# Kernel optimization log

Hardware: AMD Instinct MI355X
Metric: run time of the kernel (lower is better)

The kernel has to match this reference:

```python
import jax, jax.numpy as jnp
import numpy as np

B, T, F, D, H, DFF, L = 8, 1024, 64, 512, 8, 2048, 3
DH = D // H
PERIODS = np.array([16, 256, 4096], np.int32)
CMS_LRS = np.array([0.01, 0.001, 0.0001], np.float32)
TITANS_LR = 0.01
TITANS_CLIP = 0.1


def layernorm(x, w, b):
    m = x.mean(-1, keepdims=True)
    v = x.var(-1, keepdims=True)
    return (x - m) * jax.lax.rsqrt(v + 1e-5) * w + b


def setup_inputs() -> dict:
    key = jax.random.key(0)
    ks = jax.random.split(key, 40)
    f32 = jnp.float32
    def rn(i, shape, s=0.02):
        return jax.random.normal(ks[i], shape, f32) * s
    inp = {
        'x': jax.random.normal(ks[0], (B, T, F), f32),
        'titans_W': jnp.zeros((D, D), f32),
        'cms_summary': jnp.zeros((L, D), f32),
        'cms_buf_sum': jnp.zeros((L, D), f32),
        'cms_count': jnp.zeros((L,), jnp.int32),
        'cms_step': jnp.zeros((L,), jnp.int32),
        'in_norm_w': jnp.ones((F,), f32), 'in_norm_b': jnp.zeros((F,), f32),
        'in_proj_W': rn(1, (D, F)), 'in_proj_b': jnp.zeros((D,), f32),
        'W_base': rn(2, (D, D), 0.01),
        'tit_out_W': rn(3, (D, D)), 'tit_out_b': jnp.zeros((D,), f32),
        'gate_W': rn(4, (L, D, D)), 'gate_b': jnp.zeros((L, D), f32),
        'comb_W': rn(5, (D, L * D)), 'comb_b': jnp.zeros((D,), f32),
        'n1_w': jnp.ones((D,), f32), 'n1_b': jnp.zeros((D,), f32),
        'qkv_W': rn(6, (3 * D, D)), 'qkv_b': jnp.zeros((3 * D,), f32),
        'ao_W': rn(7, (D, D)), 'ao_b': jnp.zeros((D,), f32),
        'n2_w': jnp.ones((D,), f32), 'n2_b': jnp.zeros((D,), f32),
        'f1_W': rn(8, (DFF, D)), 'f1_b': jnp.zeros((DFF,), f32),
        'f2_W': rn(9, (D, DFF)), 'f2_b': jnp.zeros((D,), f32),
        'fn_w': jnp.ones((D,), f32), 'fn_b': jnp.zeros((D,), f32),
        'head_W': rn(10, (1, D)), 'head_b': jnp.zeros((1,), f32),
    }
    return inp


def cms_tick_all(means, summary, buf_sum, count, step, gate_W, gate_b):
    """Sequential tick over T timesteps, vectorized over the L levels.
    means: [T, D] batch-mean of final hidden at each timestep."""
    periods = jnp.asarray(PERIODS)
    lrs = jnp.asarray(CMS_LRS)
    def step_fn(carry, m):
        summ, bs, cnt, stp = carry
        bs = bs + m[None, :]              # [L, D]
        cnt = cnt + 1
        stp = stp + 1
        fire = cnt >= periods              # [L]
        acc = bs / cnt.astype(bs.dtype)[:, None]
        g = jax.nn.sigmoid(jnp.einsum('lij,lj->li', gate_W, acc) + gate_b)
        new_summ = jnp.where(fire[:, None], (1.0 - lrs)[:, None] * summ + lrs[:, None] * g * acc, summ)
        bs = jnp.where(fire[:, None], jnp.zeros_like(bs), bs)
        cnt = jnp.where(fire, jnp.zeros_like(cnt), cnt)
        return (new_summ, bs, cnt, stp), None
    (summary, buf_sum, count, step), _ = jax.lax.scan(step_fn, (summary, buf_sum, count, step), means)
    return summary, buf_sum, count, step


def reference(x, titans_W, cms_summary, cms_buf_sum, cms_count, cms_step,
              in_norm_w, in_norm_b, in_proj_W, in_proj_b,
              W_base, tit_out_W, tit_out_b,
              gate_W, gate_b, comb_W, comb_b,
              n1_w, n1_b, qkv_W, qkv_b, ao_W, ao_b,
              n2_w, n2_b, f1_W, f1_b, f2_W, f2_b,
              fn_w, fn_b, head_W, head_b):
    # input norm + projection: [B,T,F] -> [B,T,D]
    h = layernorm(x, in_norm_w, in_norm_b) @ in_proj_W.T + in_proj_b
    # Titans fast-weight read
    W = W_base + titans_W
    tit = (h @ W.T) @ tit_out_W.T + tit_out_b
    # Titans fast-weight update (detached in the original)
    hs = jax.lax.stop_gradient(h)
    target = hs.mean(axis=1)               # [B, D]
    query = hs[:, -1, :]                   # [B, D]
    pred_m = query @ titans_W.T
    err = (target - pred_m).mean(axis=0)   # [D]
    grad = jnp.outer(err, query.mean(axis=0))
    gn = jnp.linalg.norm(grad)
    grad = jnp.where(gn > TITANS_CLIP, grad * (TITANS_CLIP / gn), grad)
    new_W = titans_W + TITANS_LR * grad
    h = h + tit
    # CMS residual from current summaries: concat [L*D] -> combine -> [D]
    cms_out = cms_summary.reshape(L * D) @ comb_W.T + comb_b
    h = h + cms_out                        # broadcast over [B,T,D]
    # transformer block (pre-norm, causal MHA)
    hn = layernorm(h, n1_w, n1_b)
    qkv = hn @ qkv_W.T + qkv_b
    q, k, v = jnp.split(qkv, 3, axis=-1)
    def to_heads(t):
        return t.reshape(B, T, H, DH).transpose(0, 2, 1, 3)
    q, k, v = to_heads(q), to_heads(k), to_heads(v)
    scores = jnp.einsum('bhqd,bhkd->bhqk', q, k) / np.sqrt(DH).astype(np.float32)
    causal = jnp.triu(jnp.ones((T, T), bool), 1)
    scores = jnp.where(causal, -jnp.inf, scores)
    attn = jax.nn.softmax(scores, axis=-1)
    ao = jnp.einsum('bhqk,bhkd->bhqd', attn, v).transpose(0, 2, 1, 3).reshape(B, T, D)
    h = h + ao @ ao_W.T + ao_b
    hn2 = layernorm(h, n2_w, n2_b)
    h = h + jax.nn.gelu(hn2 @ f1_W.T + f1_b, approximate=False) @ f2_W.T + f2_b
    h = layernorm(h, fn_w, fn_b)
    pred = (h @ head_W.T + head_b).squeeze(-1)   # [B, T]
    # CMS tick over all T steps (detached in the original)
    means = jax.lax.stop_gradient(h).mean(axis=0)  # [T, D]
    ns, nb, nc, nt = cms_tick_all(means, cms_summary, cms_buf_sum, cms_count, cms_step, gate_W, gate_b)
    return pred, new_W, ns, nb, nc, nt
```

## Files before the change

### kernel.cpp

```cpp
#include <hip/hip_runtime.h>
#include <hip/hip_bf16.h>
#include <math.h>

#define Bdim 8
#define Tdim 1024
#define Fdim 64
#define Ddim 512
#define Lcms 3

#define OFF_PRED 0
#define OFF_W    8192
#define OFF_NS   270336
#define OFF_NB   271872
#define OFF_NC   273408
#define OFF_NT   273411

typedef __hip_bfloat16 bf16;
typedef __attribute__((ext_vector_type(8))) short s8;
typedef __attribute__((ext_vector_type(4))) float f4;

__device__ __forceinline__ float b2f(bf16 v){ return __bfloat162float(v); }
__device__ __forceinline__ bf16  f2b(float v){ return __float2bfloat16(v); }
__device__ __forceinline__ short fb16(float v){ bf16 t = __float2bfloat16(v); return *reinterpret_cast<short*>(&t); }
__device__ __forceinline__ float sh2f(short s){ bf16 t = *reinterpret_cast<bf16*>(&s); return __bfloat162float(t); }
__device__ __forceinline__ float toF(float v){ return v; }
__device__ __forceinline__ float toF(bf16 v){ return __bfloat162float(v); }
template<typename T> __device__ __forceinline__ T fromF(float v);
template<> __device__ __forceinline__ float fromF<float>(float v){ return v; }
template<> __device__ __forceinline__ bf16  fromF<bf16 >(float v){ return f2b(v); }

__device__ __forceinline__ f4 mfma16(s8 a, s8 b, f4 c){
  return __builtin_amdgcn_mfma_f32_16x16x32_bf16(a, b, c, 0, 0, 0);
}

__device__ __forceinline__ void gload16(const bf16* g, bf16* l){
  __builtin_amdgcn_global_load_lds(
      (const __attribute__((address_space(1))) unsigned*)g,
      (__attribute__((address_space(3))) unsigned*)l, 16, 0, 0);
}

__device__ __forceinline__ float gelu_fast(float x){
  float z2 = 1.5957691216f*(x + 0.044715f*x*x*x);
  z2 = fminf(fmaxf(z2, -18.f), 18.f);
  return x / (1.f + __expf(-z2));
}

template<typename TW>
__device__ __forceinline__ void front_misc(int blk, int tid,
    const TW* x, const TW* nw, const TW* nb_, bf16* xn,
    const TW* Wbse, const TW* tW, bf16* Wout,
    const TW* summ, const TW* combW, const TW* combb, float* outv){
  if (blk < 2048){
    int row = blk*4 + (tid>>6);
    int lane = tid & 63;
    float v = toF(x[(size_t)row*Fdim + lane]);
    float s = v, s2 = v*v;
    #pragma unroll
    for (int off=32; off; off>>=1){ s += __shfl_down(s,off); s2 += __shfl_down(s2,off); }
    s = __shfl(s, 0); s2 = __shfl(s2, 0);
    float mu = s*(1.f/64.f);
    float var = s2*(1.f/64.f) - mu*mu;
    float rstd = rsqrtf(var + 1e-5f);
    xn[(size_t)row*Fdim + lane] = f2b((v-mu)*rstd*toF(nw[lane]) + toF(nb_[lane]));
  } else if (blk < 3072){
    int i = (blk-2048)*256 + tid;
    Wout[i] = f2b(toF(Wbse[i]) + toF(tW[i]));
  } else {
    __shared__ float s_s[Lcms*Ddim];
    for (int i=tid;i<Lcms*Ddim;i+=256) s_s[i] = toF(summ[i]);
    __syncthreads();
    int wave = tid>>6, lane = tid&63;
    int d = (blk-3072)*4 + wave;
    const TW* wr = combW + (size_t)d*(Lcms*Ddim);
    float a = 0.f;
    for (int j=lane;j<Lcms*Ddim;j+=64) a += s_s[j]*toF(wr[j]);
    #pragma unroll
    for (int off=32; off; off>>=1) a += __shfl_down(a,off);
    if (lane==0) outv[d] = a + toF(combb[d]);
  }
}
__global__ __launch_bounds__(256) void k_front(
    const void* s0, const void* s1, const void* s2, const void* s3,
    const void* s4, const void* s5, const void* s6, const void* s7,
    const void* s8v, const void* s9, const void* s10, const void* s11,
    const void* s12, const void* s13,
    bf16* __restrict__ dst, const unsigned* __restrict__ w1, int* __restrict__ flag,
    const int* __restrict__ cnt, int* __restrict__ params,
    const void* x, const void* nw, const void* nb_, bf16* xn,
    const void* Wbse, const void* tW, bf16* Wout,
    const void* summ, const void* combW, const void* combb, float* outv,
    float* __restrict__ colsum){
  bool isbf = (w1[0] == 0x3F803F80u);
  int blk = blockIdx.x, tid = threadIdx.x;
  if (blk==0 && tid==0){
    flag[0] = isbf ? 1 : 0;
    const int P[3] = {16,256,4096};
    for (int l=0;l<3;l++){
      int c0 = cnt[l];
      int t1 = P[l] - c0 - 1; if (t1 < 0) t1 = 0;
      int K = (t1 >= Tdim) ? 0 : 1 + (Tdim-1-t1)/P[l];
      params[l*4+0]=t1; params[l*4+1]=K; params[l*4+2]=c0+t1+1; params[l*4+3]=c0;
    }
  }
  if (blk == 1){
    for (int i=tid; i<Bdim*Ddim; i+=256) colsum[i] = 0.f;
  }
  if (blk < 1024){
    const void* srcs[14] = {s0,s1,s2,s3,s4,s5,s6,s7,s8v,s9,s10,s11,s12,s13};
    const int   ns[14]   = {262144,512,786432,1536,262144,512,1048576,2048,1048576,512,
                            32768,512,786432,1536};
    const int gstride = 1024*256;
    int gid = blk*256 + tid;
    int base = 0;
    #pragma unroll
    for (int s=0;s<14;s++){
      int n = ns[s];
      if (isbf){
        const short* sp = (const short*)srcs[s]; short* dp = (short*)(dst+base);
        for (int i=gid;i<n;i+=gstride) dp[i] = sp[i];
      } else {
        const float* sp = (const float*)srcs[s];
        for (int i=gid;i<n;i+=gstride) dst[base+i] = f2b(sp[i]);
      }
      base += n;
    }
  } else {
    int b2 = blk - 1024;
    if (isbf) front_misc<bf16>(b2, tid, (const bf16*)x,(const bf16*)nw,(const bf16*)nb_,xn,
                               (const bf16*)Wbse,(const bf16*)tW,Wout,
                               (const bf16*)summ,(const bf16*)combW,(const bf16*)combb,outv);
    else      front_misc<float>(b2, tid, (const float*)x,(const float*)nw,(const float*)nb_,xn,
                               (const float*)Wbse,(const float*)tW,Wout,
                               (const float*)summ,(const float*)combW,(const float*)combb,outv);
  }
}

__global__ void k_tq2(const bf16* __restrict__ h, const float* __restrict__ colsum,
    float* __restrict__ target, float* __restrict__ query){
  int i = blockIdx.x*256 + threadIdx.x;
  int b = i>>9, d = i&511;
  target[i] = colsum[i]*(1.f/(float)Tdim);
  query[i]  = b2f(h[((size_t)b*Tdim + (Tdim-1))*Ddim + d]);
}

template<typename TW>
__device__ __forceinline__ void titans_err_impl(const float* target, const float* query,
    const TW* tW, float* err, float* qmean){
  int wave = threadIdx.x>>6, lane = threadIdx.x&63;
  int d = blockIdx.x*4 + wave;
  const TW* wr = tW + (size_t)d*Ddim;
  float s = 0.f;
  #pragma unroll
  for (int b=0;b<Bdim;b++){
    const float* q = query + b*Ddim;
    float p = 0.f;
    for (int j=lane;j<Ddim;j+=64) p += q[j]*toF(wr[j]);
    s += p;
  }
  #pragma unroll
  for (int off=32; off; off>>=1) s += __shfl_down(s,off);
  if (lane==0){
    float e=0.f, qm=0.f;
    #pragma unroll
    for (int b=0;b<Bdim;b++){ e += target[b*Ddim+d]; qm += query[b*Ddim+d]; }
    err[d]   = (e - s)*(1.f/(float)Bdim);
    qmean[d] = qm*(1.f/(float)Bdim);
  }
}
__global__ __launch_bounds__(256) void k_titans_err(const float* target, const float* query,
    const void* tW, float* err, float* qmean, const int* flg){
  if (*flg) titans_err_impl<bf16>(target,query,(const bf16*)tW,err,qmean);
  else      titans_err_impl<float>(target,query,(const float*)tW,err,qmean);
}

template<typename TW>
__device__ __forceinline__ void new_W_impl(const TW* tW, const float* err, const float* qmean,
    TW* outW){
  int tid = threadIdx.x;
  float a = err[tid]*err[tid] + err[tid+256]*err[tid+256];
  float b = qmean[tid]*qmean[tid] + qmean[tid+256]*qmean[tid+256];
  #pragma unroll
  for (int off=32; off; off>>=1){ a += __shfl_down(a,off); b += __shfl_down(b,off); }
  __shared__ float sa[4], sb[4];
  int lane = tid & 63, wid = tid >> 6;
  if (lane==0){ sa[wid]=a; sb[wid]=b; }
  __syncthreads();
  float A = sa[0]+sa[1]+sa[2]+sa[3];
  float Bq= sb[0]+sb[1]+sb[2]+sb[3];
  float gn = sqrtf(A*Bq);
  float sf = 0.01f * (gn > 0.1f ? 0.1f/gn : 1.0f);
  int i = blockIdx.x*256 + tid;
  int r = i >> 9, c = i & 511;
  outW[i] = fromF<TW>(toF(tW[i]) + sf*err[r]*qmean[c]);
}
__global__ __launch_bounds__(256) void k_new_W(const void* tW, const float* err,
    const float* qmean, void* out, const int* flg){
  if (*flg) new_W_impl<bf16>((const bf16*)tW, err, qmean, ((bf16*)out)+OFF_W);
  else      new_W_impl<float>((const float*)tW, err, qmean, ((float*)out)+OFF_W);
}

template<int MODE, int DEPTH>
__global__ __launch_bounds__(512) void gemm_mfma(const bf16* __restrict__ A,
    const bf16* __restrict__ Bw, const bf16* __restrict__ bias,
    const float* __restrict__ colvec, bf16* __restrict__ Cout,
    const bf16* __restrict__ resid, int M, int N, int K, float* __restrict__ colsum){
  __shared__ __align__(16) bf16 As[DEPTH][128*32];
  __shared__ __align__(16) bf16 Bs[DEPTH][128*32];
  int tid = threadIdx.x, wave = tid>>6, lane = tid&63, quad = lane>>4, l16 = lane&15;
  int row0 = blockIdx.x*128, col0 = blockIdx.y*128;
  int wr = (wave>>2)*64, wc = (wave&3)*32;
  int srow = wave*16 + (lane>>2);
  int scol = (((lane&3) ^ ((lane>>3)&3)))*8;
  int rswz = (quad ^ ((l16>>1)&3))*8;
  f4 acc[8] = {};
  int niter = K >> 5;
  #define STAGE(bu, k0) { \
    gload16(A  + (size_t)(row0 + srow)*K + (k0) + scol, &As[bu][wave*512 + lane*8]); \
    gload16(Bw + (size_t)(col0 + srow)*K + (k0) + scol, &Bs[bu][wave*512 + lane*8]); \
  }
  STAGE(0, 0)
  if (DEPTH >= 3 && niter > 1) STAGE(1, 32)
  if (DEPTH >= 4 && niter > 2) STAGE(2, 64)
  for (int k=0; k<niter; k++){
    int bu = k & (DEPTH-1);
    if (DEPTH == 2){
      if (k+1 < niter){
        STAGE((k+1)&1, (k+1)<<5)
        asm volatile("s_waitcnt vmcnt(2)" ::: "memory");
      } else {
        asm volatile("s_waitcnt vmcnt(0)" ::: "memory");
      }
    } else {
      if (k+3 < niter){
        STAGE((k+3)&3, (k+3)<<5)
        asm volatile("s_waitcnt vmcnt(6)" ::: "memory");
      } else if (k+2 < niter){
        asm volatile("s_waitcnt vmcnt(4)" ::: "memory");
      } else if (k+1 < niter){
        asm volatile("s_waitcnt vmcnt(2)" ::: "memory");
      } else {
        asm volatile("s_waitcnt vmcnt(0)" ::: "memory");
      }
    }
    __builtin_amdgcn_s_barrier();
    s8 af[4], bfv[2];
    #pragma unroll
    for (int i=0;i<4;i++) af[i]  = *reinterpret_cast<const s8*>(&As[bu][(wr + i*16 + l16)*32 + rswz]);
    #pragma unroll
    for (int j=0;j<2;j++) bfv[j] = *reinterpret_cast<const s8*>(&Bs[bu][(wc + j*16 + l16)*32 + rswz]);
    #pragma unroll
    for (int i=0;i<4;i++)
      #pragma unroll
      for (int j=0;j<2;j++)
        acc[i*2+j] = mfma16(af[i], bfv[j], acc[i*2+j]);
    asm volatile("s_waitcnt lgkmcnt(0)" ::: "memory");
    __builtin_amdgcn_s_barrier();
  }
  #undef STAGE
  float cs[2] = {0.f, 0.f};
  #pragma unroll
  for (int i=0;i<4;i++){
    #pragma unroll
    for (int j=0;j<2;j++){
      int n = col0 + wc + j*16 + l16;
      f4 a = acc[i*2+j];
      #pragma unroll
      for (int r=0;r<4;r++){
        int m = row0 + wr + i*16 + quad*4 + r;
        float v = a[r];
        if (MODE & 1) v += b2f(bias[n]);
        if (MODE & 8) v += colvec[n];
        if (MODE & 4) v = gelu_fast(v);
        if (MODE & 2) v += b2f(resid[(size_t)m*Ddim + n]);
        Cout[(size_t)m*N + n] = f2b(v);
        if (MODE & 16) cs[j] += v;
      }
    }
  }
  if (MODE & 16){
    int bIdx = blockIdx.x >> 3;
    #pragma unroll
    for (int j=0;j<2;j++){
      float c = cs[j];
      c += __shfl_xor(c, 16);
      c += __shfl_xor(c, 32);
      if (quad == 0)
        atomicAdd(&colsum[bIdx*Ddim + col0 + wc + j*16 + l16], c);
    }
  }
}

template<typename TW>
__device__ __forceinline__ void ln_impl(const bf16* in, const TW* w, const TW* b, bf16* outp){
  int row = blockIdx.x;
  const bf16* r = in + (size_t)row*Ddim;
  int tid = threadIdx.x;
  float v0 = b2f(r[tid]), v1 = b2f(r[tid + 256]);
  float s = v0+v1, s2 = v0*v0 + v1*v1;
  #pragma unroll
  for (int off=32; off; off>>=1){ s += __shfl_down(s,off); s2 += __shfl_down(s2,off); }
  __shared__ float sa[4], sb[4];
  int lane = tid & 63, wid = tid >> 6;
  if (lane==0){ sa[wid]=s; sb[wid]=s2; }
  __syncthreads();
  float ts  = sa[0]+sa[1]+sa[2]+sa[3];
  float ts2 = sb[0]+sb[1]+sb[2]+sb[3];
  float mu = ts*(1.f/(float)Ddim);
  float var = ts2*(1.f/(float)Ddim) - mu*mu;
  float rstd = rsqrtf(var + 1e-5f);
  outp[(size_t)row*Ddim + tid]       = f2b((v0-mu)*rstd*toF(w[tid])     + toF(b[tid]));
  outp[(size_t)row*Ddim + tid + 256] = f2b((v1-mu)*rstd*toF(w[tid+256]) + toF(b[tid+256]));
}
__global__ __launch_bounds__(256) void k_ln(const bf16* in, const void* w, const void* b,
    bf16* outp, const int* flg){
  if (*flg) ln_impl<bf16>(in,(const bf16*)w,(const bf16*)b,outp);
  else      ln_impl<float>(in,(const float*)w,(const float*)b,outp);
}

template<typename TW>
__device__ __forceinline__ void ln_hm_impl(const bf16* in, const TW* w, const TW* b,
    bf16* outp, const TW* hw, const TW* hb, TW* pred, float* means){
  int t = blockIdx.x;
  int tid = threadIdx.x, wave = tid>>6, lane = tid&63;
  int d0 = lane*8;
  __shared__ float msum[4][Ddim];
  float wv[8], bv[8], hwv[8];
  #pragma unroll
  for (int j=0;j<8;j++){ wv[j]=toF(w[d0+j]); bv[j]=toF(b[d0+j]); hwv[j]=toF(hw[d0+j]); }
  float hb0 = toF(hb[0]);
  float osum[8] = {0,0,0,0,0,0,0,0};
  #pragma unroll
  for (int rr=0; rr<2; rr++){
    int bb = wave*2 + rr;
    size_t row = (size_t)bb*Tdim + t;
    s8 raw = *reinterpret_cast<const s8*>(in + row*Ddim + d0);
    float v[8];
    float s=0.f, s2=0.f;
    #pragma unroll
    for (int j=0;j<8;j++){ v[j]=sh2f(raw[j]); s+=v[j]; s2+=v[j]*v[j]; }
    #pragma unroll
    for (int off=32; off; off>>=1){ s += __shfl_down(s,off); s2 += __shfl_down(s2,off); }
    s = __shfl(s,0); s2 = __shfl(s2,0);
    float mu = s*(1.f/(float)Ddim);
    float var = s2*(1.f/(float)Ddim) - mu*mu;
    float rstd = rsqrtf(var + 1e-5f);
    float sp = 0.f;
    s8 ob;
    #pragma unroll
    for (int j=0;j<8;j++){
      float o = (v[j]-mu)*rstd*wv[j] + bv[j];
      ob[j] = fb16(o);
      sp += o*hwv[j];
      osum[j] += o;
    }
    *reinterpret_cast<s8*>(outp + row*Ddim + d0) = ob;
    #pragma unroll
    for (int off=32; off; off>>=1) sp += __shfl_down(sp,off);
    if (lane==0) pred[row] = fromF<TW>(sp + hb0);
  }
  #pragma unroll
  for (int j=0;j<8;j++) msum[wave][d0+j] = osum[j];
  __syncthreads();
  for (int d=tid; d<Ddim; d+=256)
    means[(size_t)t*Ddim + d] = (msum[0][d]+msum[1][d]+msum[2][d]+msum[3][d])*(1.f/8.f);
}
__global__ __launch_bounds__(256) void k_ln_hm(const bf16* in, const void* w, const void* b,
    bf16* outp, const void* hw, const void* hb, void* out, float* means, const int* flg){
  if (*flg) ln_hm_impl<bf16>(in,(const bf16*)w,(const bf16*)b,outp,
                             (const bf16*)hw,(const bf16*)hb,((bf16*)out)+OFF_PRED,means);
  else      ln_hm_impl<float>(in,(const float*)w,(const float*)b,outp,
                             (const float*)hw,(const float*)hb,((float*)out)+OFF_PRED,means);
}

__global__ __launch_bounds__(256) void k_attn_mfma(const bf16* __restrict__ qkv,
                                                   bf16* __restrict__ ao){
  int blk = blockIdx.x;
  int bh = blk & 63;
  int qt = 15 - (blk >> 6);
  int head = bh & 7, b = bh >> 3;
  __shared__ __align__(16) bf16 Ks[2][64][72];
  __shared__ __align__(16) unsigned Vt4[2][64*36];
  __shared__ __align__(16) bf16 Ps[4][16][72];
  int tid = threadIdx.x, wave = tid>>6, lane = tid&63, quad = lane>>4, l16 = lane&15;
  int q0w = qt*64 + wave*16;
  const bf16* basep = qkv + (size_t)b*Tdim*1536 + head*64;
  s8 qf0 = *reinterpret_cast<const s8*>(basep + (size_t)(q0w+l16)*1536 + quad*8);
  s8 qf1 = *reinterpret_cast<const s8*>(basep + (size_t)(q0w+l16)*1536 + 32 + quad*8);
  f4 o[4] = {{0,0,0,0},{0,0,0,0},{0,0,0,0},{0,0,0,0}};
  float m_r[4] = {-3.0e38f,-3.0e38f,-3.0e38f,-3.0e38f};
  float l_r[4] = {0.f,0.f,0.f,0.f};
  int key_s = tid>>3, dgk = (tid&7)*8;
  int vp = tid>>3, dgv = (tid&7)*8;
  int vu4 = (((vp>>2) ^ (tid&7)) & 7)*4 + (vp&3);
  int nch = qt + 1;
  s8 kr0[2], kr1[2], vra[2], vrb[2];
  {
    const bf16* kp = basep + (size_t)key_s*1536 + 512 + dgk;
    kr0[0] = *reinterpret_cast<const s8*>(kp);
    kr1[0] = *reinterpret_cast<const s8*>(kp + (size_t)32*1536);
    const bf16* vpa = basep + (size_t)(2*vp)*1536 + 1024 + dgv;
    vra[0] = *reinterpret_cast<const s8*>(vpa);
    vrb[0] = *reinterpret_cast<const s8*>(vpa + 1536);
    if (1 < nch){
      const bf16* kp1 = basep + (size_t)(64+key_s)*1536 + 512 + dgk;
      kr0[1] = *reinterpret_cast<const s8*>(kp1);
      kr1[1] = *reinterpret_cast<const s8*>(kp1 + (size_t)32*1536);
      const bf16* vpa1 = basep + (size_t)(64 + 2*vp)*1536 + 1024 + dgv;
      vra[1] = *reinterpret_cast<const s8*>(vpa1);
      vrb[1] = *reinterpret_cast<const s8*>(vpa1 + 1536);
    }
  }
  auto do_chunk = [&](int ch, int bu){
    f4 sc4[4] = {{0,0,0,0},{0,0,0,0},{0,0,0,0},{0,0,0,0}};
    #pragma unroll
    for (int t=0;t<4;t++){
      sc4[t] = mfma16(qf0, *reinterpret_cast<const s8*>(&Ks[bu][t*16+l16][quad*8]),    sc4[t]);
      sc4[t] = mfma16(qf1, *reinterpret_cast<const s8*>(&Ks[bu][t*16+l16][32+quad*8]), sc4[t]);
    }
    int key0 = ch*64 + l16;
    #pragma unroll
    for (int r=0;r<4;r++){
      int qrow = q0w + quad*4 + r;
      float a0 = (key0      <= qrow) ? sc4[0][r]*0.125f : -3.0e38f;
      float a1 = (key0 + 16 <= qrow) ? sc4[1][r]*0.125f : -3.0e38f;
      float a2 = (key0 + 32 <= qrow) ? sc4[2][r]*0.125f : -3.0e38f;
      float a3 = (key0 + 48 <= qrow) ? sc4[3][r]*0.125f : -3.0e38f;
      float mx = fmaxf(fmaxf(a0,a1), fmaxf(a2,a3));
      mx = fmaxf(mx, __shfl_xor(mx,1)); mx = fmaxf(mx, __shfl_xor(mx,2));
      mx = fmaxf(mx, __shfl_xor(mx,4)); mx = fmaxf(mx, __shfl_xor(mx,8));
      float mnew = fmaxf(m_r[r], mx);
      float al = __expf(m_r[r]-mnew); m_r[r] = mnew;
      float p0 = __expf(a0-mnew), p1 = __expf(a1-mnew);
      float p2 = __expf(a2-mnew), p3 = __expf(a3-mnew);
      float rs = (p0+p1)+(p2+p3);
      rs += __shfl_xor(rs,1); rs += __shfl_xor(rs,2);
      rs += __shfl_xor(rs,4); rs += __shfl_xor(rs,8);
      l_r[r] = l_r[r]*al + rs;
      o[0][r]*=al; o[1][r]*=al; o[2][r]*=al; o[3][r]*=al;
      int prow = quad*4+r;
      *reinterpret_cast<short*>(&Ps[wave][prow][l16])    = fb16(p0);
      *reinterpret_cast<short*>(&Ps[wave][prow][16+l16]) = fb16(p1);
      *reinterpret_cast<short*>(&Ps[wave][prow][32+l16]) = fb16(p2);
      *reinterpret_cast<short*>(&Ps[wave][prow][48+l16]) = fb16(p3);
    }
    asm volatile("s_waitcnt lgkmcnt(0)" ::: "memory");
    s8 pf0 = *reinterpret_cast<const s8*>(&Ps[wave][l16][quad*8]);
    s8 pf1 = *reinterpret_cast<const s8*>(&Ps[wave][l16][32+quad*8]);
    #pragma unroll
    for (int j=0;j<4;j++){
      int d = j*16 + l16;
      int swz = (d>>3) & 7;
      s8 b0 = *reinterpret_cast<const s8*>(&Vt4[bu][d*36 + ((quad   ^ swz))*4]);
      s8 b1 = *reinterpret_cast<const s8*>(&Vt4[bu][d*36 + (((4+quad)^ swz))*4]);
      o[j] = mfma16(pf0, b0, o[j]);
      o[j] = mfma16(pf1, b1, o[j]);
    }
  };
  for (int ch0=0; ch0<nch; ch0+=2){
    #pragma unroll
    for (int s=0;s<2;s++){
      if (ch0+s < nch){
        *reinterpret_cast<s8*>(&Ks[s][key_s][dgk])    = kr0[s];
        *reinterpret_cast<s8*>(&Ks[s][32+key_s][dgk]) = kr1[s];
        #pragma unroll
        for (int j=0;j<8;j++){
          unsigned w = (unsigned)(unsigned short)vra[s][j] | ((unsigned)(unsigned short)vrb[s][j] << 16);
          Vt4[s][(dgv+j)*36 + vu4] = w;
        }
      }
    }
    __syncthreads();
    #pragma unroll
    for (int s=0;s<2;s++){
      int chn = ch0 + 2 + s;
      if (chn < nch){
        const bf16* kp = basep + (size_t)(chn*64+key_s)*1536 + 512 + dgk;
        kr0[s] = *reinterpret_cast<const s8*>(kp);
        kr1[s] = *reinterpret_cast<const s8*>(kp + (size_t)32*1536);
        const bf16* vpa = basep + (size_t)(chn*64 + 2*vp)*1536 + 1024 + dgv;
        vra[s] = *reinterpret_cast<const s8*>(vpa);
        vrb[s] = *reinterpret_cast<const s8*>(vpa + 1536);
      }
    }
    do_chunk(ch0, 0);
    if (ch0+1 < nch) do_chunk(ch0+1, 1);
    if (ch0+2 < nch) __syncthreads();
  }
  #pragma unroll
  for (int r=0;r<4;r++){
    float inv = 1.f/l_r[r];
    size_t rowb = (size_t)(b*Tdim + q0w + quad*4 + r)*Ddim + head*64;
    ao[rowb + l16]      = f2b(o[0][r]*inv);
    ao[rowb + 16 + l16] = f2b(o[1][r]*inv);
    ao[rowb + 32 + l16] = f2b(o[2][r]*inv);
    ao[rowb + 48 + l16] = f2b(o[3][r]*inv);
  }
}

template<typename TW>
__device__ __forceinline__ void cms_acc_impl(const float* means, const TW* bs0,
    const int* params, float* acc, bf16* acch, float* tailtmp){
  int tid = threadIdx.x;
  if (blockIdx.x < 384){
    int l = blockIdx.x>>7, k = blockIdx.x&127;
    int K = params[l*4+1];
    if (k >= K){
      for (int d=tid; d<Ddim; d+=256) acch[((size_t)l*128+k)*Ddim + d] = f2b(0.f);
      return;
    }
    int t1 = params[l*4], cnt0 = params[l*4+2];
    const int P[3] = {16,256,4096};
    int lo = (k==0) ? 0 : t1 + (k-1)*P[l] + 1;
    int hi = t1 + k*P[l];
    float inv = 1.f/((k==0) ? (float)cnt0 : (float)P[l]);
    int lane = tid&63, strip = tid>>6;
    __shared__ float red[4][Ddim];
    float4 a0 = {0,0,0,0}, a1 = {0,0,0,0};
    for (int t=lo+strip; t<=hi; t+=4){
      const float4* row = (const float4*)(means + (size_t)t*Ddim);
      float4 v0 = row[lane], v1 = row[lane+64];
      a0.x+=v0.x; a0.y+=v0.y; a0.z+=v0.z; a0.w+=v0.w;
      a1.x+=v1.x; a1.y+=v1.y; a1.z+=v1.z; a1.w+=v1.w;
    }
    ((float4*)red[strip])[lane]    = a0;
    ((float4*)red[strip])[lane+64] = a1;
    __syncthreads();
    for (int d=tid; d<Ddim; d+=256){
      float s = red[0][d]+red[1][d]+red[2][d]+red[3][d];
      if (k==0) s += toF(bs0[l*Ddim+d]);
      float v = s*inv;
      acc[((size_t)l*65+k)*Ddim + d] = v;
      acch[((size_t)l*128+k)*Ddim + d] = f2b(v);
    }
  } else {
    int bb = blockIdx.x - 384;
    int l = bb>>5, chunk = bb&31;
    int t1 = params[l*4], K = params[l*4+1];
    const int P[3] = {16,256,4096};
    int lo = (K==0) ? 0 : t1 + (K-1)*P[l] + 1;
    int f = tid & 127, strip = tid >> 7;
    int tbeg = chunk*32, tend = tbeg + 32;
    if (tbeg < lo) tbeg = lo;
    float4 a = {0,0,0,0};
    for (int t=tbeg+strip; t<tend; t+=2){
      float4 v = ((const float4*)(means + (size_t)t*Ddim))[f];
      a.x+=v.x; a.y+=v.y; a.z+=v.z; a.w+=v.w;
    }
    __shared__ float4 redt[2][128];
    redt[strip][f] = a;
    __syncthreads();
    if (strip==0){
      float4 b = redt[1][f];
      a.x+=b.x; a.y+=b.y; a.z+=b.z; a.w+=b.w;
      ((float4*)(tailtmp + ((size_t)l*32 + chunk)*Ddim))[f] = a;
    }
  }
}
__global__ __launch_bounds__(256) void k_cms_acc(const float* means, const void* bs0,
    const int* params, float* acc, bf16* acch, float* tailtmp, const int* flg){
  if (*flg) cms_acc_impl<bf16>(means,(const bf16*)bs0,params,acc,acch,tailtmp);
  else      cms_acc_impl<float>(means,(const float*)bs0,params,acc,acch,tailtmp);
}

__global__ __launch_bounds__(256) void k_cms_gate_mfma(const bf16* __restrict__ accbh,
    const bf16* __restrict__ wg, const bf16* __restrict__ wgb, float* __restrict__ g){
  int l = blockIdx.y;
  const bf16* A  = accbh + (size_t)l*128*Ddim;
  const bf16* Bw = wg    + (size_t)l*Ddim*Ddim;
  __shared__ __align__(16) bf16 As[128*32];
  __shared__ __align__(16) bf16 Bs[128*32];
  int tid = threadIdx.x, wave = tid>>6, lane = tid&63, quad = lane>>4, l16 = lane&15;
  int col0 = blockIdx.x*128;
  int wr = (wave>>1)*64, wc = (wave&1)*64;
  int srow = lane>>2, scol = (lane&3)*8;
  f4 acc[16] = {};
  for (int k0=0; k0<Ddim; k0+=32){
    __syncthreads();
    #pragma unroll
    for (int it=0; it<2; it++){
      int c = wave*2 + it;
      gload16(A  + (size_t)(c*16 + srow)*Ddim + k0 + scol, &As[c*512 + lane*8]);
      gload16(Bw + (size_t)(col0 + c*16 + srow)*Ddim + k0 + scol, &Bs[c*512 + lane*8]);
    }
    __syncthreads();
    s8 af[4], bfv[4];
    #pragma unroll
    for (int i=0;i<4;i++) af[i]  = *reinterpret_cast<const s8*>(&As[(wr + i*16 + l16)*32 + quad*8]);
    #pragma unroll
    for (int j=0;j<4;j++) bfv[j] = *reinterpret_cast<const s8*>(&Bs[(wc + j*16 + l16)*32 + quad*8]);
    #pragma unroll
    for (int i=0;i<4;i++)
      #pragma unroll
      for (int j=0;j<4;j++)
        acc[i*4+j] = mfma16(af[i], bfv[j], acc[i*4+j]);
  }
  #pragma unroll
  for (int i=0;i<4;i++){
    #pragma unroll
    for (int j=0;j<4;j++){
      int n = col0 + wc + j*16 + l16;
      f4 a = acc[i*4+j];
      #pragma unroll
      for (int r=0;r<4;r++){
        int m = wr + i*16 + quad*4 + r;
        if (m < 65){
          float v = a[r] + b2f(wgb[l*Ddim + n]);
          g[((size_t)l*65 + m)*Ddim + n] = 1.f/(1.f + __expf(-v));
        }
      }
    }
  }
}

template<typename TW>
__device__ __forceinline__ void cms_final_impl(const float* acc, const float* g,
    const float* tailtmp, const TW* summ0, const TW* bs0, const int* params,
    const int* step0, TW* out){
  int l = blockIdx.x;
  int t1 = params[l*4], K = params[l*4+1], c0 = params[l*4+3];
  const int P[3] = {16,256,4096};
  const float LR[3] = {0.01f,0.001f,0.0001f};
  float lr = LR[l];
  for (int d=threadIdx.x; d<Ddim; d+=256){
    float s = toF(summ0[l*Ddim + d]);
    for (int k=0;k<K;k++)
      s = (1.f-lr)*s + lr*g[((size_t)l*65+k)*Ddim+d]*acc[((size_t)l*65+k)*Ddim+d];
    out[OFF_NS + l*Ddim + d] = fromF<TW>(s);
    float nbv = (K==0) ? toF(bs0[l*Ddim+d]) : 0.f;
    #pragma unroll
    for (int c=0;c<32;c++) nbv += tailtmp[((size_t)l*32+c)*Ddim + d];
    out[OFF_NB + l*Ddim + d] = fromF<TW>(nbv);
  }
  if (threadIdx.x==0){
    int nc = (K==0) ? c0 + Tdim : (Tdim-1 - (t1 + (K-1)*P[l]));
    out[OFF_NC + l] = fromF<TW>((float)nc);
    out[OFF_NT + l] = fromF<TW>((float)(step0[l] + Tdim));
  }
}
__global__ __launch_bounds__(256) void k_cms_final(const float* acc, const float* g,
    const float* tailtmp, const void* summ0, const void* bs0, const int* params,
    const int* step0, void* out, const int* flg){
  if (*flg) cms_final_impl<bf16>(acc,g,tailtmp,(const bf16*)summ0,(const bf16*)bs0,params,step0,(bf16*)out);
  else      cms_final_impl<float>(acc,g,tailtmp,(const float*)summ0,(const float*)bs0,params,step0,(float*)out);
}

extern "C" void kernel_launch(void* const* d_in, const int* in_sizes, int n_in,
                              void* d_out, int out_size, void* d_ws, size_t ws_size,
                              hipStream_t stream) {
  (void)in_sizes; (void)n_in; (void)out_size; (void)ws_size;
  const void* x           = d_in[0];
  const void* titansW     = d_in[1];
  const void* cms_summary = d_in[2];
  const void* cms_bufsum  = d_in[3];
  const int*  cms_count   = (const int*)d_in[4];
  const int*  cms_step    = (const int*)d_in[5];
  const void* in_norm_w   = d_in[6];
  const void* in_norm_b   = d_in[7];
  const void* in_proj_W   = d_in[8];
  const void* in_proj_b   = d_in[9];
  const void* W_base      = d_in[10];
  const void* tit_out_W   = d_in[11];
  const void* tit_out_b   = d_in[12];
  const void* gate_W      = d_in[13];
  const void* gate_b      = d_in[14];
  const void* comb_W      = d_in[15];
  const void* comb_b      = d_in[16];
  const void* n1_w        = d_in[17];
  const void* n1_b        = d_in[18];
  const void* qkv_W       = d_in[19];
  const void* qkv_b       = d_in[20];
  const void* ao_W        = d_in[21];
  const void* ao_b        = d_in[22];
  const void* n2_w        = d_in[23];
  const void* n2_b        = d_in[24];
  const void* f1_W        = d_in[25];
  const void* f1_b        = d_in[26];
  const void* f2_W        = d_in[27];
  const void* f2_b        = d_in[28];
  const void* fn_w        = d_in[29];
  const void* fn_b        = d_in[30];
  const void* head_W      = d_in[31];
  const void* head_b      = d_in[32];

  char* u8 = (char*)d_ws;
  bf16*  h     = (bf16*)(u8 + 0);
  bf16*  hnA   = (bf16*)(u8 + 8388608);
  bf16*  big   = (bf16*)(u8 + 16777216);
  bf16*  xn    = big;
  bf16*  tmid  = big + (size_t)8192*1536;
  float* means = (float*)(u8 + 50331648);
  bf16*  Wb    = (bf16*)(u8 + 52428800);
  bf16*  wall  = (bf16*)(u8 + 52953088);
  bf16*  wtit  = wall;
  bf16*  wtitb = wall + 262144;
  bf16*  wqkv  = wall + 262656;
  bf16*  wqkvb = wall + 1049088;
  bf16*  wao   = wall + 1050624;
  bf16*  waob  = wall + 1312768;
  bf16*  wf1   = wall + 1313280;
  bf16*  wf1b  = wall + 2361856;
  bf16*  wf2   = wall + 2363904;
  bf16*  wf2b  = wall + 3412480;
  bf16*  wproj = wall + 3412992;
  bf16*  wprojb= wall + 3445760;
  bf16*  wgate = wall + 3446272;
  bf16*  wgateb= wall + 4232704;
  float* target= (float*)(u8 + 61421568);
  float* query = (float*)(u8 + 61437952);
  float* errv  = (float*)(u8 + 61454336);
  float* qmean = (float*)(u8 + 61456384);
  float* cmsout= (float*)(u8 + 61458944);
  float* accb  = (float*)(u8 + 61460992);
  float* gbuf  = (float*)(u8 + 61860352);
  bf16*  accbh = (bf16*) (u8 + 62259712);
  int*   params= (int*)  (u8 + 62652928);
  int*   dflag = (int*)  (u8 + 62652992);
  float* colsum= (float*)(u8 + 62659584);
  float* tailtmp=(float*)(u8 + 63183872);

  k_front<<<4224, 256, 0, stream>>>(tit_out_W, tit_out_b, qkv_W, qkv_b, ao_W, ao_b,
                                    f1_W, f1_b, f2_W, f2_b, in_proj_W, in_proj_b,
                                    gate_W, gate_b, wall, (const unsigned*)in_norm_w,
                                    dflag, cms_count, params,
                                    x, in_norm_w, in_norm_b, xn,
                                    W_base, titansW, Wb,
                                    cms_summary, comb_W, comb_b, cmsout, colsum);
  gemm_mfma<17,2><<<dim3(64,4), 512, 0, stream>>>(xn, wproj, wprojb, nullptr, h, nullptr, 8192, 512, 64, colsum);
  k_tq2<<<16, 256, 0, stream>>>(h, colsum, target, query);
  k_titans_err<<<128, 256, 0, stream>>>(target, query, titansW, errv, qmean, dflag);
  k_new_W<<<1024, 256, 0, stream>>>(titansW, errv, qmean, d_out, dflag);
  gemm_mfma<0,4><<<dim3(64,4), 512, 0, stream>>>(h, Wb, nullptr, nullptr, tmid, nullptr, 8192, 512, 512, nullptr);
  gemm_mfma<11,4><<<dim3(64,4), 512, 0, stream>>>(tmid, wtit, wtitb, cmsout, h, h, 8192, 512, 512, nullptr);
  k_ln<<<8192, 256, 0, stream>>>(h, n1_w, n1_b, hnA, dflag);
  gemm_mfma<1,2><<<dim3(64,12), 512, 0, stream>>>(hnA, wqkv, wqkvb, nullptr, big, nullptr, 8192, 1536, 512, nullptr);
  k_attn_mfma<<<1024, 256, 0, stream>>>(big, tmid);
  gemm_mfma<3,4><<<dim3(64,4), 512, 0, stream>>>(tmid, wao, waob, nullptr, h, h, 8192, 512, 512, nullptr);
  k_ln<<<8192, 256, 0, stream>>>(h, n2_w, n2_b, hnA, dflag);
  gemm_mfma<5,2><<<dim3(64,16), 512, 0, stream>>>(hnA, wf1, wf1b, nullptr, big, nullptr, 8192, 2048, 512, nullptr);
  gemm_mfma<3,4><<<dim3(64,4), 512, 0, stream>>>(big, wf2, wf2b, nullptr, h, h, 8192, 512, 2048, nullptr);
  k_ln_hm<<<1024, 256, 0, stream>>>(h, fn_w, fn_b, hnA, head_W, head_b, d_out, means, dflag);
  k_cms_acc<<<480, 256, 0, stream>>>(means, cms_bufsum, params, accb, accbh, tailtmp, dflag);
  k_cms_gate_mfma<<<dim3(4,3), 256, 0, stream>>>(accbh, wgate, wgateb, gbuf);
  k_cms_final<<<Lcms, 256, 0, stream>>>(accb, gbuf, tailtmp, cms_summary, cms_bufsum, params, cms_step, d_out, dflag);
}
```

Measured before the change: 432.0 us.

## Add 64-row-tile GEMM for N=512 layers and fold tq2 into titans_err

Adds a new MFMA GEMM kernel with 64x128 block tiles and double-buffered LDS staging. It is used for the four N=512 GEMMs, launching 512 blocks instead of 256 so more of the GPU's compute units are busy. It also removes the small k_tq2 kernel and lets titans_err read the last-timestep rows of h and colsum directly, saving one launch and a round trip through memory. The smaller tiles mean less operand reuse per block and more total global loads.

```diff
diff --git a/kernel.cpp b/kernel.cpp
--- a/kernel.cpp
+++ b/kernel.cpp
@@ -135,16 +135,8 @@
   }
 }
 
-__global__ void k_tq2(const bf16* __restrict__ h, const float* __restrict__ colsum,
-    float* __restrict__ target, float* __restrict__ query){
-  int i = blockIdx.x*256 + threadIdx.x;
-  int b = i>>9, d = i&511;
-  target[i] = colsum[i]*(1.f/(float)Tdim);
-  query[i]  = b2f(h[((size_t)b*Tdim + (Tdim-1))*Ddim + d]);
-}
-
 template<typename TW>
-__device__ __forceinline__ void titans_err_impl(const float* target, const float* query,
+__device__ __forceinline__ void titans_err_impl(const bf16* h, const float* colsum,
     const TW* tW, float* err, float* qmean){
   int wave = threadIdx.x>>6, lane = threadIdx.x&63;
   int d = blockIdx.x*4 + wave;
@@ -152,9 +144,9 @@
   float s = 0.f;
   #pragma unroll
   for (int b=0;b<Bdim;b++){
-    const float* q = query + b*Ddim;
+    const bf16* q = h + ((size_t)b*Tdim + (Tdim-1))*Ddim;
     float p = 0.f;
-    for (int j=lane;j<Ddim;j+=64) p += q[j]*toF(wr[j]);
+    for (int j=lane;j<Ddim;j+=64) p += b2f(q[j])*toF(wr[j]);
     s += p;
   }
   #pragma unroll
@@ -162,15 +154,18 @@
   if (lane==0){
     float e=0.f, qm=0.f;
     #pragma unroll
-    for (int b=0;b<Bdim;b++){ e += target[b*Ddim+d]; qm += query[b*Ddim+d]; }
+    for (int b=0;b<Bdim;b++){
+      e  += colsum[b*Ddim+d]*(1.f/(float)Tdim);
+      qm += b2f(h[((size_t)b*Tdim + (Tdim-1))*Ddim + d]);
+    }
     err[d]   = (e - s)*(1.f/(float)Bdim);
     qmean[d] = qm*(1.f/(float)Bdim);
   }
 }
-__global__ __launch_bounds__(256) void k_titans_err(const float* target, const float* query,
+__global__ __launch_bounds__(256) void k_titans_err(const bf16* h, const float* colsum,
     const void* tW, float* err, float* qmean, const int* flg){
-  if (*flg) titans_err_impl<bf16>(target,query,(const bf16*)tW,err,qmean);
-  else      titans_err_impl<float>(target,query,(const float*)tW,err,qmean);
+  if (*flg) titans_err_impl<bf16>(h,colsum,(const bf16*)tW,err,qmean);
+  else      titans_err_impl<float>(h,colsum,(const float*)tW,err,qmean);
 }
 
 template<typename TW>
@@ -286,6 +281,71 @@
       c += __shfl_xor(c, 32);
       if (quad == 0)
         atomicAdd(&colsum[bIdx*Ddim + col0 + wc + j*16 + l16], c);
+    }
+  }
+}
+
+template<int MODE>
+__global__ __launch_bounds__(512) void gemm_mfma64(const bf16* __restrict__ A,
+    const bf16* __restrict__ Bw, const bf16* __restrict__ bias,
+    const float* __restrict__ colvec, bf16* __restrict__ Cout,
+    const bf16* __restrict__ resid, int M, int N, int K){
+  __shared__ __align__(16) bf16 As[2][64*32];
+  __shared__ __align__(16) bf16 Bs[2][128*32];
+  int tid = threadIdx.x, wave = tid>>6, lane = tid&63, quad = lane>>4, l16 = lane&15;
+  int row0 = blockIdx.x*64, col0 = blockIdx.y*128;
+  int wr = (wave>>2)*32, wc = (wave&3)*32;
+  int srow = lane>>2;
+  int scol = (((lane&3) ^ ((lane>>3)&3)))*8;
+  int rswz = (quad ^ ((l16>>1)&3))*8;
+  f4 acc[4] = {};
+  int niter = K >> 5;
+  #define STAGE64(bu, k0) { \
+    if (wave < 4) \
+      gload16(A + (size_t)(row0 + wave*16 + srow)*K + (k0) + scol, &As[bu][wave*512 + lane*8]); \
+    gload16(Bw + (size_t)(col0 + wave*16 + srow)*K + (k0) + scol, &Bs[bu][wave*512 + lane*8]); \
+  }
+  STAGE64(0, 0)
+  for (int k=0; k<niter; k++){
+    int bu = k & 1;
+    if (k+1 < niter){
+      STAGE64((k+1)&1, (k+1)<<5)
+      if (wave < 4) asm volatile("s_waitcnt vmcnt(2)" ::: "memory");
+      else          asm volatile("s_waitcnt vmcnt(1)" ::: "memory");
+    } else {
+      asm volatile("s_waitcnt vmcnt(0)" ::: "memory");
+    }
+    __builtin_amdgcn_s_barrier();
+    s8 af[2], bfv[2];
+    #pragma unroll
+    for (int i=0;i<2;i++) af[i]  = *reinterpret_cast<const s8*>(&As[bu][(wr + i*16 + l16)*32 + rswz]);
+    #pragma unroll
+    for (int j=0;j<2;j++) bfv[j] = *reinterpret_cast<const s8*>(&Bs[bu][(wc + j*16 + l16)*32 + rswz]);
+    #pragma unroll
+    for (int i=0;i<2;i++)
+      #pragma unroll
+      for (int j=0;j<2;j++)
+        acc[i*2+j] = mfma16(af[i], bfv[j], acc[i*2+j]);
+    asm volatile("s_waitcnt lgkmcnt(0)" ::: "memory");
+    __builtin_amdgcn_s_barrier();
+  }
+  #undef STAGE64
+  #pragma unroll
+  for (int i=0;i<2;i++){
+    #pragma unroll
+    for (int j=0;j<2;j++){
+      int n = col0 + wc + j*16 + l16;
+      f4 a = acc[i*2+j];
+      #pragma unroll
+      for (int r=0;r<4;r++){
+        int m = row0 + wr + i*16 + quad*4 + r;
+        float v = a[r];
+        if (MODE & 1) v += b2f(bias[n]);
+        if (MODE & 8) v += colvec[n];
+        if (MODE & 4) v = gelu_fast(v);
+        if (MODE & 2) v += b2f(resid[(size_t)m*Ddim + n]);
+        Cout[(size_t)m*N + n] = f2b(v);
+      }
     }
   }
 }
@@ -705,8 +765,6 @@
   bf16*  wprojb= wall + 3445760;
   bf16*  wgate = wall + 3446272;
   bf16*  wgateb= wall + 4232704;
-  float* target= (float*)(u8 + 61421568);
-  float* query = (float*)(u8 + 61437952);
   float* errv  = (float*)(u8 + 61454336);
   float* qmean = (float*)(u8 + 61456384);
   float* cmsout= (float*)(u8 + 61458944);
@@ -726,18 +784,17 @@
                                     W_base, titansW, Wb,
                                     cms_summary, comb_W, comb_b, cmsout, colsum);
   gemm_mfma<17,2><<<dim3(64,4), 512, 0, stream>>>(xn, wproj, wprojb, nullptr, h, nullptr, 8192, 512, 64, colsum);
-  k_tq2<<<16, 256, 0, stream>>>(h, colsum, target, query);
-  k_titans_err<<<128, 256, 0, stream>>>(target, query, titansW, errv, qmean, dflag);
+  k_titans_err<<<128, 256, 0, stream>>>(h, colsum, titansW, errv, qmean, dflag);
   k_new_W<<<1024, 256, 0, stream>>>(titansW, errv, qmean, d_out, dflag);
-  gemm_mfma<0,4><<<dim3(64,4), 512, 0, stream>>>(h, Wb, nullptr, nullptr, tmid, nullptr, 8192, 512, 512, nullptr);
-  gemm_mfma<11,4><<<dim3(64,4), 512, 0, stream>>>(tmid, wtit, wtitb, cmsout, h, h, 8192, 512, 512, nullptr);
+  gemm_mfma64<0><<<dim3(128,4), 512, 0, stream>>>(h, Wb, nullptr, nullptr, tmid, nullptr, 8192, 512, 512);
+  gemm_mfma64<11><<<dim3(128,4), 512, 0, stream>>>(tmid, wtit, wtitb, cmsout, h, h, 8192, 512, 512);
   k_ln<<<8192, 256, 0, stream>>>(h, n1_w, n1_b, hnA, dflag);
   gemm_mfma<1,2><<<dim3(64,12), 512, 0, stream>>>(hnA, wqkv, wqkvb, nullptr, big, nullptr, 8192, 1536, 512, nullptr);
   k_attn_mfma<<<1024, 256, 0, stream>>>(big, tmid);
-  gemm_mfma<3,4><<<dim3(64,4), 512, 0, stream>>>(tmid, wao, waob, nullptr, h, h, 8192, 512, 512, nullptr);
+  gemm_mfma64<3><<<dim3(128,4), 512, 0, stream>>>(tmid, wao, waob, nullptr, h, h, 8192, 512, 512);
   k_ln<<<8192, 256, 0, stream>>>(h, n2_w, n2_b, hnA, dflag);
   gemm_mfma<5,2><<<dim3(64,16), 512, 0, stream>>>(hnA, wf1, wf1b, nullptr, big, nullptr, 8192, 2048, 512, nullptr);
-  gemm_mfma<3,4><<<dim3(64,4), 512, 0, stream>>>(big, wf2, wf2b, nullptr, h, h, 8192, 512, 2048, nullptr);
+  gemm_mfma64<3><<<dim3(128,4), 512, 0, stream>>>(big, wf2, wf2b, nullptr, h, h, 8192, 512, 2048);
   k_ln_hm<<<1024, 256, 0, stream>>>(h, fn_w, fn_b, hnA, head_W, head_b, d_out, means, dflag);
   k_cms_acc<<<480, 256, 0, stream>>>(means, cms_bufsum, params, accb, accbh, tailtmp, dflag);
   k_cms_gate_mfma<<<dim3(4,3), 256, 0, stream>>>(accbh, wgate, wgateb, gbuf);
```

New measurement: 419.7 us (median of 3 runs). 1.03x faster.
